# Kernel tuning notes

Hardware: AMD Instinct MI355X
Metric: run time of the kernel (lower is better)

Reference implementation:

```python
import jax, jax.numpy as jnp
import numpy as np

H = 32  # rnn/encoder/residual hidden dim
NEG = -1e9


def gru(x, h0, Wih, Whh, bih, bhh):
    # x: (B,T,D), h0: (B,H); torch GRU gate order [r,z,n]
    xp = jnp.swapaxes(x @ Wih.T + bih, 0, 1)  # (T,B,3H)

    def step(h, xt):
        gh = h @ Whh.T + bhh
        xr, xz, xn = jnp.split(xt, 3, axis=-1)
        hr, hz, hn = jnp.split(gh, 3, axis=-1)
        r = jax.nn.sigmoid(xr + hr)
        z = jax.nn.sigmoid(xz + hz)
        n = jnp.tanh(xn + r * hn)
        h_new = (1.0 - z) * n + z * h
        return h_new, h_new

    hT, ys = jax.lax.scan(step, h0, xp)
    return jnp.swapaxes(ys, 0, 1), hT  # (B,T,H), (B,H)


def setup_inputs():
    key = jax.random.key(0)
    ks = jax.random.split(key, 30)
    B, T = 2048, 128
    def lin(k, o, i):
        return jax.random.normal(k, (o, i), jnp.float32) / np.sqrt(i)
    inp = {}
    inp['obs'] = jax.random.normal(ks[0], (B, T, 15), jnp.float32)
    inp['rnn_state'] = jax.random.normal(ks[1], (1, B, 3 * H), jnp.float32)
    inp['enc_air_W'] = lin(ks[2], H, 7); inp['enc_air_b'] = jnp.zeros((H,), jnp.float32)
    inp['enc_m_W'] = lin(ks[3], H, 4); inp['enc_m_b'] = jnp.zeros((H,), jnp.float32)
    inp['air_Wih'] = lin(ks[4], 3 * H, H); inp['air_Whh'] = lin(ks[5], 3 * H, H)
    inp['air_bih'] = jnp.zeros((3 * H,), jnp.float32); inp['air_bhh'] = jnp.zeros((3 * H,), jnp.float32)
    inp['m_Wih'] = lin(ks[6], 3 * H, H); inp['m_Whh'] = lin(ks[7], 3 * H, H)
    inp['m_bih'] = jnp.zeros((3 * H,), jnp.float32); inp['m_bhh'] = jnp.zeros((3 * H,), jnp.float32)
    inp['attn_in_w'] = lin(ks[8], 3 * H, H); inp['attn_in_b'] = jnp.zeros((3 * H,), jnp.float32)
    inp['attn_out_w'] = lin(ks[9], H, H); inp['attn_out_b'] = jnp.zeros((H,), jnp.float32)
    inp['mlp_W0'] = lin(ks[10], 256, 2 * H); inp['mlp_b0'] = jnp.zeros((256,), jnp.float32)
    inp['mlp_W1'] = lin(ks[11], 256, 256); inp['mlp_b1'] = jnp.zeros((256,), jnp.float32)
    inp['out_W'] = lin(ks[12], 1, 256); inp['out_b'] = jnp.zeros((1,), jnp.float32)
    return inp


def reference(obs, rnn_state, enc_air_W, enc_air_b, enc_m_W, enc_m_b,
              air_Wih, air_Whh, air_bih, air_bhh,
              m_Wih, m_Whh, m_bih, m_bhh,
              attn_in_w, attn_in_b, attn_out_w, attn_out_b,
              mlp_W0, mlp_b0, mlp_W1, mlp_b1, out_W, out_b):
    B, T, _ = obs.shape
    h_air0 = rnn_state[0, :, :H]                       # (B,H)
    h_m0 = rnn_state[0, :, H:].reshape(2 * B, H)       # faithful reshape (1,B,64)->(1,2B,32)

    # aircraft branch
    air_emb = obs[..., 8:] @ enc_air_W.T + enc_air_b   # (B,T,H)
    air_feat, next_h_air = gru(air_emb, h_air0, air_Wih, air_Whh, air_bih, air_bhh)

    # missile branch: concat missiles along batch dim
    m_raw = jnp.concatenate([obs[..., 0:4], obs[..., 4:8]], axis=0)  # (2B,T,4)
    m_emb = m_raw @ enc_m_W.T + enc_m_b
    m_feat, next_h_m = gru(m_emb, h_m0, m_Wih, m_Whh, m_bih, m_bhh)
    m1_feat, m2_feat = m_feat[:B], m_feat[B:]

    # inactive-missile mask from raw obs
    obs_flat = obs.reshape(-1, 15)
    inact = jnp.array([1.0, 0.0, 1.0, 0.0], jnp.float32)
    mask = jnp.stack([
        jnp.all(jnp.isclose(obs_flat[:, 0:4], inact), axis=-1),
        jnp.all(jnp.isclose(obs_flat[:, 4:8], inact), axis=-1),
    ], axis=1)                                          # (N,2) True = masked

    N = B * T
    air_flat = air_feat.reshape(N, H)
    m1_flat = m1_feat.reshape(N, H)
    m2_flat = m2_feat.reshape(N, H)

    # 2-head attention, q len 1, kv len 2
    Wq, Wk, Wv = jnp.split(attn_in_w, 3, axis=0)
    bq, bk, bv = jnp.split(attn_in_b, 3, axis=0)
    nh, hd = 2, H // 2
    qh = (air_flat @ Wq.T + bq).reshape(N, nh, hd)
    kv = jnp.stack([m1_flat, m2_flat], axis=1)          # (N,2,H)
    kh = (kv @ Wk.T + bk).reshape(N, 2, nh, hd)
    vh = (kv @ Wv.T + bv).reshape(N, 2, nh, hd)
    scores = jnp.einsum('nhd,nkhd->nhk', qh, kh) / np.sqrt(hd)
    scores = scores + jnp.where(mask[:, None, :], NEG, 0.0)
    w = jax.nn.softmax(scores, axis=-1)
    ctx = jnp.einsum('nhk,nkhd->nhd', w, vh).reshape(N, H)
    attn = ctx @ attn_out_w.T + attn_out_b
    attn = jnp.where(jnp.all(mask, axis=-1, keepdims=True), 0.0, attn)  # torch nan_to_num(all-masked)

    fusion = jnp.concatenate([air_flat, attn], axis=-1)  # (N,2H)
    h1 = jax.nn.leaky_relu(fusion @ mlp_W0.T + mlp_b0, 0.01)
    h2 = jax.nn.leaky_relu(h1 @ mlp_W1.T + mlp_b1, 0.01)
    val = h2 @ out_W.T + out_b                           # (N,1)

    next_h = jnp.concatenate([next_h_air, next_h_m.reshape(B, 2 * H)], axis=-1)[None]  # (1,B,96)
    return val, next_h
```

## Files before the change

### kernel.cpp

```cpp
#include <hip/hip_runtime.h>
#include <hip/hip_bf16.h>

#define BB 2048
#define TT 128
#define NN (BB*TT)
#define NVAL NN

#define OFF_BCA   768u
#define OFF_BCM   1632u
#define OFF_W0P   2048u
#define OFF_W1P   10240u
#define OFF_WQKV  43008u
#define OFF_WO    44544u
#define OFF_WH2A  45568u
#define OFF_WH2M  47104u
#define OFF_WC2A  48640u
#define OFF_WC2M  49024u
#define OFF_AIRF  83968u
#define OFF_MF    4278272u
#define OFF_MASK  12666880u

typedef __attribute__((ext_vector_type(8))) short short8;
typedef __attribute__((ext_vector_type(4))) float f32x4;
typedef _Float16 h2 __attribute__((ext_vector_type(2)));

__device__ __forceinline__ unsigned short f2bf(float f) {
    unsigned u = __builtin_bit_cast(unsigned, f);
    u += 0x7FFFu + ((u >> 16) & 1u);
    return (unsigned short)(u >> 16);
}
__device__ __forceinline__ unsigned f2h(float f) {
    _Float16 h = (_Float16)f;
    return (unsigned)__builtin_bit_cast(unsigned short, h);
}
__device__ __forceinline__ unsigned pkh2(float a, float b) {
    return (f2h(b) << 16) | f2h(a);
}
__device__ __forceinline__ float dot2(unsigned w, unsigned x, float acc) {
    return __builtin_amdgcn_fdot2(__builtin_bit_cast(h2, w),
                                  __builtin_bit_cast(h2, x), acc, false);
}

__global__ __launch_bounds__(256) void prep_kernel(
    const float* __restrict__ enc_air_W, const float* __restrict__ enc_air_b,
    const float* __restrict__ enc_m_W,   const float* __restrict__ enc_m_b,
    const float* __restrict__ air_Wih,   const float* __restrict__ air_bih,
    const float* __restrict__ m_Wih,     const float* __restrict__ m_bih,
    const float* __restrict__ air_Whh,   const float* __restrict__ m_Whh,
    const float* __restrict__ W0,        const float* __restrict__ W1,
    const float* __restrict__ attn_in_w, const float* __restrict__ attn_out_w,
    float* __restrict__ ws)
{
    int b = blockIdx.x, t = threadIdx.x;
    if (b == 0) {
        if (t < 96) {
            float bacc = air_bih[t];
            for (int k = 0; k < 32; k++) bacc += air_Wih[t*32+k] * enc_air_b[k];
            ws[OFF_BCA + t] = bacc;
            float bacc2 = m_bih[t];
            for (int k = 0; k < 32; k++) bacc2 += m_Wih[t*32+k] * enc_m_b[k];
            ws[OFF_BCM + t] = bacc2;
        }
    } else if (b <= 32) {
        unsigned short* w1p = (unsigned short*)(ws + OFF_W1P);
        int base = ((b-1)*256 + t);
        int lane = base & 63;
        int ctf  = base >> 6;
        int ct   = ctf & 15, s = ctf >> 4;
        int col = lane & 15, quad = lane >> 4;
        int k0 = s*32 + quad*8;
        int o  = ct*16 + col;
        #pragma unroll
        for (int j = 0; j < 8; j++)
            w1p[base*8 + j] = f2bf(W1[o*256 + k0 + j]);
    } else if (b <= 40) {
        unsigned short* w0p = (unsigned short*)(ws + OFF_W0P);
        int base = ((b-33)*256 + t);
        int lane = base & 63;
        int ctf  = base >> 6;
        int ct   = ctf & 15, s = ctf >> 4;
        int col = lane & 15, quad = lane >> 4;
        int k0 = s*32 + quad*8;
        int o  = ct*16 + col;
        #pragma unroll
        for (int j = 0; j < 8; j++)
            w0p[base*8 + j] = f2bf(W0[o*64 + k0 + j]);
    } else if (b == 41) {
        unsigned short* wqkv = (unsigned short*)(ws + OFF_WQKV);
        unsigned short* wop  = (unsigned short*)(ws + OFF_WO);
        for (int slot = t; slot < 512; slot += 256) {
            if (slot < 384) {
                int ct = slot >> 6, lane = slot & 63;
                int col = lane & 15, quad = lane >> 4;
                int o = ct*16 + col;
                #pragma unroll
                for (int j = 0; j < 8; j++)
                    wqkv[slot*8 + j] = f2bf(attn_in_w[o*32 + quad*8 + j]);
            } else {
                int s2 = slot - 384;
                int ct = s2 >> 6, lane = s2 & 63;
                int col = lane & 15, quad = lane >> 4;
                #pragma unroll
                for (int j = 0; j < 8; j++)
                    wop[s2*8 + j] = f2bf(attn_out_w[(ct*16+col)*32 + quad*8 + j]);
            }
        }
    } else if (b == 42) {
        unsigned* wa = (unsigned*)(ws + OFF_WH2A);
        unsigned* wm = (unsigned*)(ws + OFF_WH2M);
        for (int s = t; s < 3072; s += 256) {
            int s2 = (s < 1536) ? s : s - 1536;
            const float* W = (s < 1536) ? air_Whh : m_Whh;
            unsigned* dst = (s < 1536) ? wa : wm;
            int o = s2 >> 4, j = s2 & 15;
            dst[s2] = pkh2(W[o*32 + 2*j], W[o*32 + 2*j + 1]);
        }
    } else {
        unsigned* wa = (unsigned*)(ws + OFF_WC2A);
        unsigned* wm = (unsigned*)(ws + OFF_WC2M);
        for (int s = t; s < 768; s += 256) {
            int s2 = (s < 384) ? s : s - 384;
            bool is_air = (s < 384);
            unsigned* dst = is_air ? wa : wm;
            int o = s2 >> 2, j = s2 & 3;
            int ni  = is_air ? 7 : 4;
            float c0 = 0.f, c1 = 0.f;
            int i0 = 2*j, i1 = 2*j + 1;
            if (i0 < ni)
                for (int k = 0; k < 32; k++)
                    c0 += (is_air ? air_Wih[o*32+k]*enc_air_W[k*7+i0]
                                  : m_Wih[o*32+k]*enc_m_W[k*4+i0]);
            if (i1 < ni)
                for (int k = 0; k < 32; k++)
                    c1 += (is_air ? air_Wih[o*32+k]*enc_air_W[k*7+i1]
                                  : m_Wih[o*32+k]*enc_m_W[k*4+i1]);
            dst[s2] = pkh2(c0, c1);
        }
    }
}

template<int NI, int NP, bool DO_MASK>
__device__ void gru_row(const float* __restrict__ in_base,
                        const unsigned* __restrict__ wc2,
                        const float* __restrict__ bc,
                        const unsigned* __restrict__ wh2,
                        const float* __restrict__ bhh,
                        float h0,
                        unsigned short* __restrict__ feat_out,
                        float* __restrict__ hT_out,
                        float* __restrict__ mask_out,
                        int lane, int half)
{
    unsigned whr[16], whz[16], whn[16];
    #pragma unroll
    for (int j = 0; j < 16; j++) {
        whr[j] = wh2[lane*16 + j];
        whz[j] = wh2[(32+lane)*16 + j];
        whn[j] = wh2[(64+lane)*16 + j];
    }
    unsigned cr2[NP], cz2[NP], cn2[NP];
    #pragma unroll
    for (int j = 0; j < NP; j++) {
        cr2[j] = wc2[lane*4 + j];
        cz2[j] = wc2[(32+lane)*4 + j];
        cn2[j] = wc2[(64+lane)*4 + j];
    }
    const float bcr = bc[lane], bcz = bc[32+lane], bcn = bc[64+lane];
    const float bhr = bhh[lane], bhz = bhh[32+lane], bhn = bhh[64+lane];

    float h = h0;
    for (int t = 0; t < TT; t++) {
        float xin = (lane < NI) ? in_base[t*15 + lane] : 0.f;

        bool ok = true;
        if (DO_MASK) {
            bool pred = true;
            if (lane < 4) {
                const float c   = ((lane & 1) == 0) ? 1.f : 0.f;
                const float thr = ((lane & 1) == 0) ? 1.00001e-5f : 1e-8f;
                pred = fabsf(xin - c) <= thr;
            }
            unsigned long long ball = __ballot(pred);
            ok = (((ball >> (half*32)) & 0xFull) == 0xFull);
        }

        unsigned x16 = f2h(xin);
        unsigned xnb = (unsigned)__shfl_xor((int)x16, 1, 32);
        unsigned xpk = (xnb << 16) | x16;

        float ar = bcr, az = bcz, an = bcn;
        #pragma unroll
        for (int j = 0; j < NP; j++) {
            unsigned px = (unsigned)__shfl((int)xpk, 2*j, 32);
            ar = dot2(cr2[j], px, ar);
            az = dot2(cz2[j], px, az);
            an = dot2(cn2[j], px, an);
        }

        unsigned h16 = f2h(h);
        unsigned hnb = (unsigned)__shfl_xor((int)h16, 1, 32);
        unsigned hpk = (hnb << 16) | h16;

        float hr = bhr, hz = bhz, hn = bhn;
        #pragma unroll
        for (int j = 0; j < 16; j++) {
            unsigned ph = (unsigned)__shfl((int)hpk, 2*j, 32);
            hr = dot2(whr[j], ph, hr);
            hz = dot2(whz[j], ph, hz);
            hn = dot2(whn[j], ph, hn);
        }

        float r = 1.f / (1.f + __expf(-(ar + hr)));
        float z = 1.f / (1.f + __expf(-(az + hz)));
        float pre = an + r*hn;
        float e2 = __expf(2.f*pre);
        float n = 1.f - 2.f/(e2 + 1.f);
        h = n + z*(h - n);

        unsigned bf = f2bf(h);
        unsigned nb = (unsigned)__shfl_xor((int)bf, 1, 32);
        if ((lane & 1) == 0)
            *(unsigned*)(feat_out + t*32 + lane) = (nb << 16) | bf;

        if (DO_MASK && lane == 0) mask_out[t*2] = ok ? 1.f : 0.f;
    }
    *hT_out = h;
}

__global__ __launch_bounds__(256) void gru_kernel(
    const float* __restrict__ obs, const float* __restrict__ rnn,
    const float* __restrict__ ws,
    const float* __restrict__ air_bhh, const float* __restrict__ m_bhh,
    unsigned short* __restrict__ air_feat, unsigned short* __restrict__ m_feat,
    float* __restrict__ mask_f, float* __restrict__ nh_out)
{
    int lane = threadIdx.x & 31;
    int half = (threadIdx.x >> 5) & 1;
    int r = blockIdx.x*8 + (threadIdx.x >> 5);
    if (r < BB) {
        const float* in_base = obs + r*(TT*15) + 8;
        float h0 = rnn[r*96 + lane];
        gru_row<7,4,false>(in_base,
                         (const unsigned*)(ws + OFF_WC2A), ws + OFF_BCA,
                         (const unsigned*)(ws + OFF_WH2A), air_bhh, h0,
                         air_feat + (size_t)r*TT*32,
                         nh_out + r*96 + lane, nullptr, lane, half);
    } else {
        int i = r - BB;
        int b = (i < BB) ? i : i - BB;
        int slot = (i < BB) ? 0 : 1;
        const float* in_base = obs + b*(TT*15) + slot*4;
        float h0 = rnn[(i >> 1)*96 + 32 + (i & 1)*32 + lane];
        gru_row<4,2,true>(in_base,
                        (const unsigned*)(ws + OFF_WC2M), ws + OFF_BCM,
                        (const unsigned*)(ws + OFF_WH2M), m_bhh, h0,
                        m_feat + (size_t)i*TT*32,
                        nh_out + (i >> 1)*96 + 32 + (i & 1)*32 + lane,
                        mask_f + (size_t)(b*TT)*2 + slot, lane, half);
    }
}

__global__ __launch_bounds__(256) void fused_kernel(
    const unsigned short* __restrict__ air_feat, const unsigned short* __restrict__ m_feat,
    const float* __restrict__ mask_f,
    const unsigned short* __restrict__ wqkv, const float* __restrict__ attn_in_b,
    const unsigned short* __restrict__ wop,  const float* __restrict__ attn_out_b,
    const unsigned short* __restrict__ w0p, const float* __restrict__ b0,
    const unsigned short* __restrict__ w1p, const float* __restrict__ b1,
    const float* __restrict__ outW, const float* __restrict__ outb,
    float* __restrict__ val)
{
    __shared__ unsigned short A1[64*72];
    __shared__ unsigned short U[64*264];
    __shared__ float MS[128];
    __shared__ float PS[4][64];

    unsigned short* AM = U;
    unsigned short* CT = U + 64*72;
    unsigned short* A2 = U;

    const int tid  = threadIdx.x;
    const int lane = tid & 63;
    const int strip = tid >> 6;
    const int col  = lane & 15;
    const int quad = lane >> 4;
    const size_t n0 = (size_t)blockIdx.x * 64;

    {
        int row = tid >> 2, c0 = (tid & 3)*8;
        short8 va  = *(const short8*)(air_feat + (n0 + row)*32 + c0);
        *(short8*)&A1[row*72 + c0] = va;
        short8 vm1 = *(const short8*)(m_feat + (n0 + row)*32 + c0);
        *(short8*)&AM[row*72 + c0] = vm1;
        short8 vm2 = *(const short8*)(m_feat + ((size_t)NN + n0 + row)*32 + c0);
        *(short8*)&AM[row*72 + 32 + c0] = vm2;
        if (tid < 128) MS[tid] = mask_f[n0*2 + tid];
    }
    __syncthreads();

    {
        short8 a_air = *(const short8*)&A1[(strip*16 + col)*72 + quad*8];
        short8 a_m1  = *(const short8*)&AM[(strip*16 + col)*72 + quad*8];
        short8 a_m2  = *(const short8*)&AM[(strip*16 + col)*72 + 32 + quad*8];

        f32x4 q[2], k1[2], k2[2], v1[2], v2[2], ao[2];
        #pragma unroll
        for (int ct = 0; ct < 2; ct++) {
            f32x4 z = (f32x4){0.f,0.f,0.f,0.f};
            short8 wqf = *(const short8*)(wqkv + ((0+ct)*64 + lane)*8);
            short8 wkf = *(const short8*)(wqkv + ((2+ct)*64 + lane)*8);
            short8 wvf = *(const short8*)(wqkv + ((4+ct)*64 + lane)*8);
            q[ct]  = __builtin_amdgcn_mfma_f32_16x16x32_bf16(a_air, wqf, z, 0,0,0);
            k1[ct] = __builtin_amdgcn_mfma_f32_16x16x32_bf16(a_m1,  wkf, z, 0,0,0);
            k2[ct] = __builtin_amdgcn_mfma_f32_16x16x32_bf16(a_m2,  wkf, z, 0,0,0);
            v1[ct] = __builtin_amdgcn_mfma_f32_16x16x32_bf16(a_m1,  wvf, z, 0,0,0);
            v2[ct] = __builtin_amdgcn_mfma_f32_16x16x32_bf16(a_m2,  wvf, z, 0,0,0);
        }
        float bqr[2], bkr[2], bvr[2];
        #pragma unroll
        for (int ct = 0; ct < 2; ct++) {
            bqr[ct] = attn_in_b[ct*16 + col];
            bkr[ct] = attn_in_b[32 + ct*16 + col];
            bvr[ct] = attn_in_b[64 + ct*16 + col];
        }
        float p1s[2][4], p2s[2][4];
        #pragma unroll
        for (int ct = 0; ct < 2; ct++) {
            #pragma unroll
            for (int reg = 0; reg < 4; reg++) {
                float qq = q[ct][reg] + bqr[ct];
                float p1 = qq * (k1[ct][reg] + bkr[ct]);
                float p2 = qq * (k2[ct][reg] + bkr[ct]);
                #pragma unroll
                for (int m = 1; m < 16; m <<= 1) {
                    p1 += __shfl_xor(p1, m, 64);
                    p2 += __shfl_xor(p2, m, 64);
                }
                p1s[ct][reg] = p1; p2s[ct][reg] = p2;
            }
        }
        float bothm[4];
        #pragma unroll
        for (int reg = 0; reg < 4; reg++) {
            int rloc = strip*16 + quad*4 + reg;
            float m0v = MS[rloc*2], m1v = MS[rloc*2 + 1];
            bothm[reg] = (m0v > 0.5f && m1v > 0.5f) ? 1.f : 0.f;
            #pragma unroll
            for (int ct = 0; ct < 2; ct++) {
                float s1 = p1s[ct][reg]*0.25f + (m0v > 0.5f ? -1e9f : 0.f);
                float s2 = p2s[ct][reg]*0.25f + (m1v > 0.5f ? -1e9f : 0.f);
                float mx = fmaxf(s1, s2);
                float e1 = __expf(s1 - mx), e2 = __expf(s2 - mx);
                float inv = 1.f/(e1 + e2);
                float ctxv = ((v1[ct][reg] + bvr[ct])*e1 +
                              (v2[ct][reg] + bvr[ct])*e2) * inv;
                CT[rloc*40 + ct*16 + col] = f2bf(ctxv);
            }
        }
        short8 a_ctx = *(const short8*)&CT[(strip*16 + col)*40 + quad*8];
        #pragma unroll
        for (int ct = 0; ct < 2; ct++) {
            f32x4 z = (f32x4){0.f,0.f,0.f,0.f};
            short8 wof = *(const short8*)(wop + (ct*64 + lane)*8);
            ao[ct] = __builtin_amdgcn_mfma_f32_16x16x32_bf16(a_ctx, wof, z, 0,0,0);
        }
        float bor[2] = { attn_out_b[col], attn_out_b[16 + col] };
        #pragma unroll
        for (int reg = 0; reg < 4; reg++) {
            int rloc = strip*16 + quad*4 + reg;
            #pragma unroll
            for (int ct = 0; ct < 2; ct++) {
                float av = ao[ct][reg] + bor[ct];
                av = (bothm[reg] > 0.5f) ? 0.f : av;
                A1[rloc*72 + 32 + ct*16 + col] = f2bf(av);
            }
        }
    }
    __syncthreads();

    float b0r[4], b1r[4], owr[4];
    #pragma unroll
    for (int c = 0; c < 4; c++) {
        int ct = strip*4 + c;
        b0r[c] = b0[ct*16 + col];
        b1r[c] = b1[ct*16 + col];
        owr[c] = outW[ct*16 + col];
    }
    const float outb0 = outb[0];

    f32x4 acc1[4][4];
    #pragma unroll
    for (int s = 0; s < 4; s++)
        #pragma unroll
        for (int c = 0; c < 4; c++) acc1[s][c] = (f32x4){0.f,0.f,0.f,0.f};
    #pragma unroll
    for (int ks = 0; ks < 2; ks++) {
        short8 a[4];
        #pragma unroll
        for (int s = 0; s < 4; s++)
            a[s] = *(const short8*)&A1[(s*16 + col)*72 + ks*32 + quad*8];
        #pragma unroll
        for (int c = 0; c < 4; c++) {
            int ct = strip*4 + c;
            short8 bfr = *(const short8*)(w0p + ((ks*16 + ct)*64 + lane)*8);
            #pragma unroll
            for (int s = 0; s < 4; s++)
                acc1[s][c] = __builtin_amdgcn_mfma_f32_16x16x32_bf16(a[s], bfr, acc1[s][c], 0, 0, 0);
        }
    }
    __syncthreads();
    #pragma unroll
    for (int s = 0; s < 4; s++) {
        #pragma unroll
        for (int c = 0; c < 4; c++) {
            int ct = strip*4 + c;
            #pragma unroll
            for (int reg = 0; reg < 4; reg++) {
                float h = acc1[s][c][reg] + b0r[c];
                h = (h > 0.f) ? h : 0.01f*h;
                A2[(s*16 + quad*4 + reg)*264 + ct*16 + col] = f2bf(h);
            }
        }
    }
    __syncthreads();

    f32x4 acc2[4][4];
    #pragma unroll
    for (int s = 0; s < 4; s++)
        #pragma unroll
        for (int c = 0; c < 4; c++) acc2[s][c] = (f32x4){0.f,0.f,0.f,0.f};
    for (int ks = 0; ks < 8; ks++) {
        short8 a[4];
        #pragma unroll
        for (int s = 0; s < 4; s++)
            a[s] = *(const short8*)&A2[(s*16 + col)*264 + ks*32 + quad*8];
        #pragma unroll
        for (int c = 0; c < 4; c++) {
            int ct = strip*4 + c;
            short8 bfr = *(const short8*)(w1p + ((ks*16 + ct)*64 + lane)*8);
            #pragma unroll
            for (int s = 0; s < 4; s++)
                acc2[s][c] = __builtin_amdgcn_mfma_f32_16x16x32_bf16(a[s], bfr, acc2[s][c], 0, 0, 0);
        }
    }

    #pragma unroll
    for (int s = 0; s < 4; s++) {
        float pv[4];
        #pragma unroll
        for (int reg = 0; reg < 4; reg++) pv[reg] = 0.f;
        #pragma unroll
        for (int c = 0; c < 4; c++) {
            #pragma unroll
            for (int reg = 0; reg < 4; reg++) {
                float h = acc2[s][c][reg] + b1r[c];
                h = (h > 0.f) ? h : 0.01f*h;
                pv[reg] += h*owr[c];
            }
        }
        #pragma unroll
        for (int reg = 0; reg < 4; reg++) {
            #pragma unroll
            for (int m = 1; m < 16; m <<= 1)
                pv[reg] += __shfl_xor(pv[reg], m, 64);
            if (col == 0) PS[strip][s*16 + quad*4 + reg] = pv[reg];
        }
    }
    __syncthreads();
    if (tid < 64)
        val[n0 + tid] = PS[0][tid] + PS[1][tid] + PS[2][tid] + PS[3][tid] + outb0;
}

extern "C" void kernel_launch(void* const* d_in, const int* in_sizes, int n_in,
                              void* d_out, int out_size, void* d_ws, size_t ws_size,
                              hipStream_t stream) {
    const float* obs        = (const float*)d_in[0];
    const float* rnn        = (const float*)d_in[1];
    const float* enc_air_W  = (const float*)d_in[2];
    const float* enc_air_b  = (const float*)d_in[3];
    const float* enc_m_W    = (const float*)d_in[4];
    const float* enc_m_b    = (const float*)d_in[5];
    const float* air_Wih    = (const float*)d_in[6];
    const float* air_Whh    = (const float*)d_in[7];
    const float* air_bih    = (const float*)d_in[8];
    const float* air_bhh    = (const float*)d_in[9];
    const float* m_Wih      = (const float*)d_in[10];
    const float* m_Whh      = (const float*)d_in[11];
    const float* m_bih      = (const float*)d_in[12];
    const float* m_bhh      = (const float*)d_in[13];
    const float* attn_in_w  = (const float*)d_in[14];
    const float* attn_in_b  = (const float*)d_in[15];
    const float* attn_out_w = (const float*)d_in[16];
    const float* attn_out_b = (const float*)d_in[17];
    const float* mlp_W0     = (const float*)d_in[18];
    const float* mlp_b0     = (const float*)d_in[19];
    const float* mlp_W1     = (const float*)d_in[20];
    const float* mlp_b1     = (const float*)d_in[21];
    const float* out_W      = (const float*)d_in[22];
    const float* out_b      = (const float*)d_in[23];

    float* ws  = (float*)d_ws;
    float* out = (float*)d_out;

    prep_kernel<<<44, 256, 0, stream>>>(enc_air_W, enc_air_b, enc_m_W, enc_m_b,
                                        air_Wih, air_bih, m_Wih, m_bih,
                                        air_Whh, m_Whh,
                                        mlp_W0, mlp_W1, attn_in_w, attn_out_w, ws);

    gru_kernel<<<768, 256, 0, stream>>>(obs, rnn, ws, air_bhh, m_bhh,
                                        (unsigned short*)(ws + OFF_AIRF),
                                        (unsigned short*)(ws + OFF_MF),
                                        ws + OFF_MASK, out + NVAL);

    fused_kernel<<<NN/64, 256, 0, stream>>>((const unsigned short*)(ws + OFF_AIRF),
                                            (const unsigned short*)(ws + OFF_MF),
                                            ws + OFF_MASK,
                                            (const unsigned short*)(ws + OFF_WQKV), attn_in_b,
                                            (const unsigned short*)(ws + OFF_WO),   attn_out_b,
                                            (const unsigned short*)(ws + OFF_W0P), mlp_b0,
                                            (const unsigned short*)(ws + OFF_W1P), mlp_b1,
                                            out_W, out_b, out);
}
```

Baseline: 326.5 us.

## Split each GRU row's K-reduction across two half-waves, one row per wave

Each GRU sequence row is now handled by a full 64-lane wavefront instead of a 32-lane half-wave. The two halves each compute half of the input and hidden dot products and combine them with a cross-half shuffle, which halves the serial per-step dot-product chain and the weight registers per lane. The input and hidden biases for r and z are folded into one constant. The grid doubles, so the whole problem now uses twice as many wavefronts, and each step pays four extra cross-half shuffles and leaves half the lanes idle during stores.

```diff
diff --git a/kernel.cpp b/kernel.cpp
--- a/kernel.cpp
+++ b/kernel.cpp
@@ -139,92 +139,99 @@
     }
 }
 
-template<int NI, int NP, bool DO_MASK>
-__device__ void gru_row(const float* __restrict__ in_base,
-                        const unsigned* __restrict__ wc2,
-                        const float* __restrict__ bc,
-                        const unsigned* __restrict__ wh2,
-                        const float* __restrict__ bhh,
-                        float h0,
-                        unsigned short* __restrict__ feat_out,
-                        float* __restrict__ hT_out,
-                        float* __restrict__ mask_out,
-                        int lane, int half)
+template<int NI, int NP2, bool DO_MASK>
+__device__ void gru_row64(const float* __restrict__ in_base,
+                          const unsigned* __restrict__ wc2,
+                          const float* __restrict__ bc,
+                          const unsigned* __restrict__ wh2,
+                          const float* __restrict__ bhh,
+                          float h0,
+                          unsigned short* __restrict__ feat_out,
+                          float* __restrict__ hT_out,
+                          float* __restrict__ mask_out,
+                          int lane)
 {
-    unsigned whr[16], whz[16], whn[16];
-    #pragma unroll
-    for (int j = 0; j < 16; j++) {
-        whr[j] = wh2[lane*16 + j];
-        whz[j] = wh2[(32+lane)*16 + j];
-        whn[j] = wh2[(64+lane)*16 + j];
-    }
-    unsigned cr2[NP], cz2[NP], cn2[NP];
-    #pragma unroll
-    for (int j = 0; j < NP; j++) {
-        cr2[j] = wc2[lane*4 + j];
-        cz2[j] = wc2[(32+lane)*4 + j];
-        cn2[j] = wc2[(64+lane)*4 + j];
-    }
-    const float bcr = bc[lane], bcz = bc[32+lane], bcn = bc[64+lane];
-    const float bhr = bhh[lane], bhz = bhh[32+lane], bhn = bhh[64+lane];
+    const int l32 = lane & 31;
+    const int sub = lane >> 5;
+
+    unsigned whr[8], whz[8], whn[8];
+    #pragma unroll
+    for (int j = 0; j < 8; j++) {
+        whr[j] = wh2[l32*16      + sub*8 + j];
+        whz[j] = wh2[(32+l32)*16 + sub*8 + j];
+        whn[j] = wh2[(64+l32)*16 + sub*8 + j];
+    }
+    unsigned cr2[NP2], cz2[NP2], cn2[NP2];
+    #pragma unroll
+    for (int j = 0; j < NP2; j++) {
+        cr2[j] = wc2[l32*4      + sub*NP2 + j];
+        cz2[j] = wc2[(32+l32)*4 + sub*NP2 + j];
+        cn2[j] = wc2[(64+l32)*4 + sub*NP2 + j];
+    }
+    const float br = bc[l32]      + bhh[l32];
+    const float bz = bc[32 + l32] + bhh[32 + l32];
+    const float bxn = bc[64 + l32];
+    const float bhn = bhh[64 + l32];
 
     float h = h0;
     for (int t = 0; t < TT; t++) {
-        float xin = (lane < NI) ? in_base[t*15 + lane] : 0.f;
+        float xin = (l32 < NI) ? in_base[t*15 + l32] : 0.f;
 
         bool ok = true;
         if (DO_MASK) {
             bool pred = true;
-            if (lane < 4) {
-                const float c   = ((lane & 1) == 0) ? 1.f : 0.f;
-                const float thr = ((lane & 1) == 0) ? 1.00001e-5f : 1e-8f;
+            if (l32 < 4) {
+                const float c   = ((l32 & 1) == 0) ? 1.f : 0.f;
+                const float thr = ((l32 & 1) == 0) ? 1.00001e-5f : 1e-8f;
                 pred = fabsf(xin - c) <= thr;
             }
             unsigned long long ball = __ballot(pred);
-            ok = (((ball >> (half*32)) & 0xFull) == 0xFull);
+            ok = ((ball & 0xFull) == 0xFull);
         }
 
         unsigned x16 = f2h(xin);
         unsigned xnb = (unsigned)__shfl_xor((int)x16, 1, 32);
         unsigned xpk = (xnb << 16) | x16;
 
-        float ar = bcr, az = bcz, an = bcn;
-        #pragma unroll
-        for (int j = 0; j < NP; j++) {
-            unsigned px = (unsigned)__shfl((int)xpk, 2*j, 32);
-            ar = dot2(cr2[j], px, ar);
-            az = dot2(cz2[j], px, az);
-            an = dot2(cn2[j], px, an);
-        }
-
         unsigned h16 = f2h(h);
         unsigned hnb = (unsigned)__shfl_xor((int)h16, 1, 32);
         unsigned hpk = (hnb << 16) | h16;
 
-        float hr = bhr, hz = bhz, hn = bhn;
-        #pragma unroll
-        for (int j = 0; j < 16; j++) {
-            unsigned ph = (unsigned)__shfl((int)hpk, 2*j, 32);
-            hr = dot2(whr[j], ph, hr);
-            hz = dot2(whz[j], ph, hz);
+        float sr = 0.f, sz = 0.f, xn = 0.f, hn = 0.f;
+        #pragma unroll
+        for (int j = 0; j < NP2; j++) {
+            unsigned px = (unsigned)__shfl((int)xpk, 2*(sub*NP2 + j), 32);
+            sr = dot2(cr2[j], px, sr);
+            sz = dot2(cz2[j], px, sz);
+            xn = dot2(cn2[j], px, xn);
+        }
+        #pragma unroll
+        for (int j = 0; j < 8; j++) {
+            unsigned ph = (unsigned)__shfl((int)hpk, 2*(sub*8 + j), 32);
+            sr = dot2(whr[j], ph, sr);
+            sz = dot2(whz[j], ph, sz);
             hn = dot2(whn[j], ph, hn);
         }
-
-        float r = 1.f / (1.f + __expf(-(ar + hr)));
-        float z = 1.f / (1.f + __expf(-(az + hz)));
-        float pre = an + r*hn;
+        sr += __shfl_xor(sr, 32, 64);
+        sz += __shfl_xor(sz, 32, 64);
+        xn += __shfl_xor(xn, 32, 64);
+        hn += __shfl_xor(hn, 32, 64);
+
+        float r = 1.f / (1.f + __expf(-(sr + br)));
+        float z = 1.f / (1.f + __expf(-(sz + bz)));
+        float pre = xn + bxn + r*(hn + bhn);
         float e2 = __expf(2.f*pre);
         float n = 1.f - 2.f/(e2 + 1.f);
         h = n + z*(h - n);
 
         unsigned bf = f2bf(h);
         unsigned nb = (unsigned)__shfl_xor((int)bf, 1, 32);
-        if ((lane & 1) == 0)
-            *(unsigned*)(feat_out + t*32 + lane) = (nb << 16) | bf;
+        if (lane < 32 && (l32 & 1) == 0)
+            *(unsigned*)(feat_out + t*32 + l32) = (nb << 16) | bf;
 
         if (DO_MASK && lane == 0) mask_out[t*2] = ok ? 1.f : 0.f;
     }
-    *hT_out = h;
+    if (lane < 32) *hT_out = h;
 }
 
 __global__ __launch_bounds__(256) void gru_kernel(
@@ -234,29 +241,29 @@
     unsigned short* __restrict__ air_feat, unsigned short* __restrict__ m_feat,
     float* __restrict__ mask_f, float* __restrict__ nh_out)
 {
-    int lane = threadIdx.x & 31;
-    int half = (threadIdx.x >> 5) & 1;
-    int r = blockIdx.x*8 + (threadIdx.x >> 5);
-    if (r < BB) {
-        const float* in_base = obs + r*(TT*15) + 8;
-        float h0 = rnn[r*96 + lane];
-        gru_row<7,4,false>(in_base,
+    int lane = threadIdx.x & 63;
+    int l32 = lane & 31;
+    int g = blockIdx.x*4 + (threadIdx.x >> 6);
+    if (g < BB) {
+        const float* in_base = obs + g*(TT*15) + 8;
+        float h0 = rnn[g*96 + l32];
+        gru_row64<7,2,false>(in_base,
                          (const unsigned*)(ws + OFF_WC2A), ws + OFF_BCA,
                          (const unsigned*)(ws + OFF_WH2A), air_bhh, h0,
-                         air_feat + (size_t)r*TT*32,
-                         nh_out + r*96 + lane, nullptr, lane, half);
+                         air_feat + (size_t)g*TT*32,
+                         nh_out + g*96 + l32, nullptr, lane);
     } else {
-        int i = r - BB;
+        int i = g - BB;
         int b = (i < BB) ? i : i - BB;
         int slot = (i < BB) ? 0 : 1;
         const float* in_base = obs + b*(TT*15) + slot*4;
-        float h0 = rnn[(i >> 1)*96 + 32 + (i & 1)*32 + lane];
-        gru_row<4,2,true>(in_base,
+        float h0 = rnn[(i >> 1)*96 + 32 + (i & 1)*32 + l32];
+        gru_row64<4,1,true>(in_base,
                         (const unsigned*)(ws + OFF_WC2M), ws + OFF_BCM,
                         (const unsigned*)(ws + OFF_WH2M), m_bhh, h0,
                         m_feat + (size_t)i*TT*32,
-                        nh_out + (i >> 1)*96 + 32 + (i & 1)*32 + lane,
-                        mask_f + (size_t)(b*TT)*2 + slot, lane, half);
+                        nh_out + (i >> 1)*96 + 32 + (i & 1)*32 + l32,
+                        mask_f + (size_t)(b*TT)*2 + slot, lane);
     }
 }
 
@@ -507,7 +514,7 @@
                                         air_Whh, m_Whh,
                                         mlp_W0, mlp_W1, attn_in_w, attn_out_w, ws);
 
-    gru_kernel<<<768, 256, 0, stream>>>(obs, rnn, ws, air_bhh, m_bhh,
+    gru_kernel<<<1536, 256, 0, stream>>>(obs, rnn, ws, air_bhh, m_bhh,
                                         (unsigned short*)(ws + OFF_AIRF),
                                         (unsigned short*)(ws + OFF_MF),
                                         ws + OFF_MASK, out + NVAL);
```

Measured after the change: 375.8 us. 1.15x slower.
